# Kernel tuning notes

Measured on AMD Instinct MI355X. Metric: run time of the kernel, lower is better.

The kernel has to match this reference:

```python
import jax, jax.numpy as jnp
import numpy as np

N, E, F, H, ED, C, G = 50000, 800000, 86, 128, 16, 18, 64
NEG_SLOPE = 0.2


def setup_inputs() -> dict:
    key = jax.random.key(0)
    ks = jax.random.split(key, 20)
    s = 0.1
    return {
        "x": jax.random.normal(ks[0], (N, F), jnp.float32),
        "edge_index": jax.random.randint(ks[1], (2, E), 0, N, jnp.int32),
        "edge_attr": jax.random.normal(ks[2], (E, ED), jnp.float32),
        "batch": jnp.sort(jax.random.randint(ks[3], (N,), 0, G, jnp.int32)),
        # conv1 params (GATConv, heads=1): lin, lin_edge (no bias), att vectors, bias
        "W1": jax.random.normal(ks[4], (F, H), jnp.float32) * s,
        "We1": jax.random.normal(ks[5], (ED, H), jnp.float32) * s,
        "as1": jax.random.normal(ks[6], (H,), jnp.float32) * s,
        "ad1": jax.random.normal(ks[7], (H,), jnp.float32) * s,
        "ae1": jax.random.normal(ks[8], (H,), jnp.float32) * s,
        "b1": jnp.zeros((H,), jnp.float32),
        # conv2 params
        "W2": jax.random.normal(ks[9], (H, H), jnp.float32) * s,
        "We2": jax.random.normal(ks[10], (ED, H), jnp.float32) * s,
        "as2": jax.random.normal(ks[11], (H,), jnp.float32) * s,
        "ad2": jax.random.normal(ks[12], (H,), jnp.float32) * s,
        "ae2": jax.random.normal(ks[13], (H,), jnp.float32) * s,
        "b2": jnp.zeros((H,), jnp.float32),
        # final classifier
        "Wl": jax.random.normal(ks[14], (H, C), jnp.float32) * s,
        "bl": jnp.zeros((C,), jnp.float32),
    }


def gat_conv(x, edge_attr, src, dst, W, We, a_src, a_dst, a_edge, bias):
    h = x @ W                                   # [N, H]
    e = edge_attr @ We                          # [E, H]
    # per-edge attention logits: a_src.h_j + a_dst.h_i + a_edge.e
    alpha = (h @ a_src)[src] + (h @ a_dst)[dst] + e @ a_edge   # [E]
    alpha = jax.nn.leaky_relu(alpha, NEG_SLOPE)
    # segment softmax over incoming edges of each destination node
    m = jax.ops.segment_max(alpha, dst, num_segments=N)
    ex = jnp.exp(alpha - m[dst])
    denom = jax.ops.segment_sum(ex, dst, num_segments=N)
    w = ex / jnp.maximum(denom[dst], 1e-16)     # [E]
    out = jax.ops.segment_sum(h[src] * w[:, None], dst, num_segments=N)
    return out + bias


def reference(x, edge_index, edge_attr, batch,
              W1, We1, as1, ad1, ae1, b1,
              W2, We2, as2, ad2, ae2, b2,
              Wl, bl):
    src, dst = edge_index[0], edge_index[1]
    h = jax.nn.relu(gat_conv(x, edge_attr, src, dst, W1, We1, as1, ad1, ae1, b1))
    h = jax.nn.relu(gat_conv(h, edge_attr, src, dst, W2, We2, as2, ad2, ae2, b2))
    pooled = jax.ops.segment_max(h, batch, num_segments=G)      # [G, H] global max pool
    pooled = jnp.where(jnp.isfinite(pooled), pooled, 0.0)       # guard empty graphs
    logits = pooled @ Wl + bl                                   # [G, C]
    return jax.nn.log_softmax(logits, axis=-1)
```

## Files before the change

### kernel.cpp

```cpp
#include <hip/hip_runtime.h>
#include <math.h>

#define N_NODES 50000
#define N_EDGES 800000
#define F_IN    86
#define H_DIM   128
#define ED_DIM  16
#define C_CLS   18
#define G_GRAPHS 64
#define NEG_SLOPE 0.2f
#define SCAN_BLOCKS ((N_NODES + 255) / 256)

typedef _Float16 h2v   __attribute__((ext_vector_type(2)));
typedef _Float16 half8 __attribute__((ext_vector_type(8)));
typedef float    f4v   __attribute__((ext_vector_type(4)));

__device__ __forceinline__ void atomicMaxFloat(float* addr, float val) {
    if (val >= 0.0f) atomicMax((int*)addr, __float_as_int(val));
    else             atomicMin((unsigned int*)addr, __float_as_uint(val));
}

__global__ void prep(int* __restrict__ cnt, float* __restrict__ pooled,
                     const float* __restrict__ We1, const float* __restrict__ ae1,
                     const float* __restrict__ We2, const float* __restrict__ ae2,
                     float* __restrict__ ve1, float* __restrict__ ve2) {
    int b = blockIdx.x, t = threadIdx.x;
    if (b < SCAN_BLOCKS) {
        int i = b * 256 + t;
        if (i < N_NODES) cnt[i] = 0;
    } else {
        if (t < ED_DIM) {
            float s = 0.f;
            for (int h = 0; h < H_DIM; ++h) s += We1[t * H_DIM + h] * ae1[h];
            ve1[t] = s;
        } else if (t < 2 * ED_DIM) {
            int j = t - ED_DIM;
            float s = 0.f;
            for (int h = 0; h < H_DIM; ++h) s += We2[j * H_DIM + h] * ae2[h];
            ve2[j] = s;
        }
        for (int i = t; i < G_GRAPHS * H_DIM; i += 256) pooled[i] = 0.f;
    }
}

__global__ void hist_rank_dots(const int* __restrict__ dst, int* __restrict__ cnt,
                               unsigned short* __restrict__ rank,
                               const float* __restrict__ ea,
                               const float* __restrict__ ve1, const float* __restrict__ ve2,
                               unsigned int* __restrict__ dotp) {
    int e = blockIdx.x * blockDim.x + threadIdx.x;
    if (e >= N_EDGES) return;
    int r = atomicAdd(&cnt[dst[e]], 1);
    rank[e] = (unsigned short)r;
    const float4* p = (const float4*)(ea + (size_t)e * ED_DIM);
    float4 v0 = p[0], v1 = p[1], v2 = p[2], v3 = p[3];
    float s1 = v0.x*ve1[0] + v0.y*ve1[1] + v0.z*ve1[2] + v0.w*ve1[3]
             + v1.x*ve1[4] + v1.y*ve1[5] + v1.z*ve1[6] + v1.w*ve1[7]
             + v2.x*ve1[8] + v2.y*ve1[9] + v2.z*ve1[10] + v2.w*ve1[11]
             + v3.x*ve1[12] + v3.y*ve1[13] + v3.z*ve1[14] + v3.w*ve1[15];
    float s2 = v0.x*ve2[0] + v0.y*ve2[1] + v0.z*ve2[2] + v0.w*ve2[3]
             + v1.x*ve2[4] + v1.y*ve2[5] + v1.z*ve2[6] + v1.w*ve2[7]
             + v2.x*ve2[8] + v2.y*ve2[9] + v2.z*ve2[10] + v2.w*ve2[11]
             + v3.x*ve2[12] + v3.y*ve2[13] + v3.z*ve2[14] + v3.w*ve2[15];
    h2v dv;
    dv.x = (_Float16)s1;
    dv.y = (_Float16)s2;
    dotp[e] = __builtin_bit_cast(unsigned int, dv);
}

__global__ void scan1(const int* __restrict__ cnt, int* __restrict__ excl,
                      int* __restrict__ bsum) {
    __shared__ int s[256];
    int tid = threadIdx.x;
    int i = blockIdx.x * 256 + tid;
    int v = (i < N_NODES) ? cnt[i] : 0;
    s[tid] = v;
    __syncthreads();
    for (int o = 1; o < 256; o <<= 1) {
        int t = (tid >= o) ? s[tid - o] : 0;
        __syncthreads();
        s[tid] += t;
        __syncthreads();
    }
    if (i < N_NODES) excl[i] = s[tid] - v;
    if (tid == 255) bsum[blockIdx.x] = s[255];
}

__global__ void scan23(const int* __restrict__ excl, const int* __restrict__ bsum,
                       int* __restrict__ row_ptr) {
    __shared__ int s[256];
    int tid = threadIdx.x;
    int v = (tid < SCAN_BLOCKS) ? bsum[tid] : 0;
    s[tid] = v;
    __syncthreads();
    for (int o = 1; o < 256; o <<= 1) {
        int t = (tid >= o) ? s[tid - o] : 0;
        __syncthreads();
        s[tid] += t;
        __syncthreads();
    }
    int boff = s[blockIdx.x] - bsum[blockIdx.x];
    int i = blockIdx.x * 256 + tid;
    if (i < N_NODES) row_ptr[i] = excl[i] + boff;
    if (i == 0) row_ptr[N_NODES] = N_EDGES;
}

__global__ void scatter_lite(const int* __restrict__ src, const int* __restrict__ dst,
                             const int* __restrict__ row_ptr,
                             const unsigned short* __restrict__ rank,
                             const unsigned int* __restrict__ dotp,
                             int2* __restrict__ perm) {
    int e = blockIdx.x * blockDim.x + threadIdx.x;
    if (e >= N_EDGES) return;
    int pos = row_ptr[dst[e]] + rank[e];
    perm[pos] = make_int2(src[e], (int)dotp[e]);
}

#define KP1 104
__global__ __launch_bounds__(256)
void gemm1(const float* __restrict__ in, const float* __restrict__ W,
           const float* __restrict__ a_s, const float* __restrict__ a_d,
           _Float16* __restrict__ hout, float* __restrict__ hs, float* __restrict__ hd) {
    __shared__ __attribute__((aligned(16))) _Float16 Asm[64 * KP1];
    __shared__ __attribute__((aligned(16))) _Float16 Bsm[128 * KP1];
    __shared__ float sdots[64][2][2];
    int tid = threadIdx.x;
    int n0 = blockIdx.x * 64;

    const float2* in2 = (const float2*)(in + (size_t)n0 * F_IN);
    for (int idx = tid; idx < 64 * (F_IN / 2); idx += 256) {
        int r = idx / (F_IN / 2), k2 = idx - r * (F_IN / 2);
        float2 v = (n0 + r < N_NODES) ? in2[idx] : make_float2(0.f, 0.f);
        Asm[r * KP1 + 2 * k2]     = (_Float16)v.x;
        Asm[r * KP1 + 2 * k2 + 1] = (_Float16)v.y;
    }
    for (int idx = tid; idx < 64 * (96 - F_IN); idx += 256) {
        int r = idx / (96 - F_IN), k = F_IN + idx - r * (96 - F_IN);
        Asm[r * KP1 + k] = (_Float16)0.f;
    }
    const float4* W4 = (const float4*)W;
    for (int idx = tid; idx < F_IN * 32; idx += 256) {
        float4 v = W4[idx];
        int k = idx >> 5, n = (idx & 31) * 4;
        Bsm[(n + 0) * KP1 + k] = (_Float16)v.x;
        Bsm[(n + 1) * KP1 + k] = (_Float16)v.y;
        Bsm[(n + 2) * KP1 + k] = (_Float16)v.z;
        Bsm[(n + 3) * KP1 + k] = (_Float16)v.w;
    }
    for (int idx = tid; idx < 128 * (96 - F_IN); idx += 256) {
        int n = idx / (96 - F_IN), k = F_IN + idx - n * (96 - F_IN);
        Bsm[n * KP1 + k] = (_Float16)0.f;
    }
    __syncthreads();

    int wave = tid >> 6, lane = tid & 63;
    int wm = (wave & 1) * 32, wn = (wave >> 1) * 64;
    int m16 = lane & 15, quad = lane >> 4;

    f4v acc[2][4];
#pragma unroll
    for (int t = 0; t < 2; ++t)
#pragma unroll
        for (int c = 0; c < 4; ++c) acc[t][c] = (f4v){0.f, 0.f, 0.f, 0.f};

#pragma unroll
    for (int kk = 0; kk < 96 / 32; ++kk) {
        int koff = kk * 32 + quad * 8;
        half8 a0 = *(const half8*)&Asm[(wm + m16) * KP1 + koff];
        half8 a1 = *(const half8*)&Asm[(wm + 16 + m16) * KP1 + koff];
#pragma unroll
        for (int c = 0; c < 4; ++c) {
            half8 b = *(const half8*)&Bsm[(wn + c * 16 + m16) * KP1 + koff];
            acc[0][c] = __builtin_amdgcn_mfma_f32_16x16x32_f16(a0, b, acc[0][c], 0, 0, 0);
            acc[1][c] = __builtin_amdgcn_mfma_f32_16x16x32_f16(a1, b, acc[1][c], 0, 0, 0);
        }
    }

    float asv[4], adv[4];
#pragma unroll
    for (int c = 0; c < 4; ++c) {
        asv[c] = a_s[wn + c * 16 + m16];
        adv[c] = a_d[wn + c * 16 + m16];
    }
#pragma unroll
    for (int t = 0; t < 2; ++t)
#pragma unroll
        for (int r = 0; r < 4; ++r) {
            float ps = 0.f, pd = 0.f;
#pragma unroll
            for (int c = 0; c < 4; ++c) {
                float v = acc[t][c][r];
                ps += v * asv[c];
                pd += v * adv[c];
            }
#pragma unroll
            for (int o = 1; o < 16; o <<= 1) {
                ps += __shfl_xor(ps, o);
                pd += __shfl_xor(pd, o);
            }
            if (m16 == 0) {
                int row = wm + t * 16 + quad * 4 + r;
                sdots[row][wn >> 6][0] = ps;
                sdots[row][wn >> 6][1] = pd;
            }
        }
#pragma unroll
    for (int t = 0; t < 2; ++t)
#pragma unroll
        for (int c = 0; c < 4; ++c)
#pragma unroll
            for (int r = 0; r < 4; ++r) {
                int row = n0 + wm + t * 16 + quad * 4 + r;
                if (row < N_NODES)
                    hout[(size_t)row * H_DIM + wn + c * 16 + m16] = (_Float16)acc[t][c][r];
            }
    __syncthreads();
    if (tid < 64) {
        int row = n0 + tid;
        if (row < N_NODES) {
            hs[row] = sdots[tid][0][0] + sdots[tid][1][0];
            hd[row] = sdots[tid][0][1] + sdots[tid][1][1];
        }
    }
}

#define KP2 136
__global__ __launch_bounds__(256)
void gemm2(const _Float16* __restrict__ in, const float* __restrict__ W,
           const float* __restrict__ a_s, const float* __restrict__ a_d,
           _Float16* __restrict__ hout, float* __restrict__ hs, float* __restrict__ hd) {
    __shared__ __attribute__((aligned(16))) _Float16 Asm[64 * KP2];
    __shared__ __attribute__((aligned(16))) _Float16 Bsm[128 * KP2];
    __shared__ float sdots[64][2][2];
    int tid = threadIdx.x;
    int n0 = blockIdx.x * 64;

    const half8* in8 = (const half8*)(in + (size_t)n0 * H_DIM);
    for (int idx = tid; idx < 64 * 16; idx += 256) {
        int r = idx >> 4, k8 = idx & 15;
        half8 v = (n0 + r < N_NODES) ? in8[idx]
                                     : (half8){0, 0, 0, 0, 0, 0, 0, 0};
        *(half8*)&Asm[r * KP2 + k8 * 8] = v;
    }
    const float4* W4 = (const float4*)W;
    for (int idx = tid; idx < 128 * 32; idx += 256) {
        float4 v = W4[idx];
        int k = idx >> 5, n = (idx & 31) * 4;
        Bsm[(n + 0) * KP2 + k] = (_Float16)v.x;
        Bsm[(n + 1) * KP2 + k] = (_Float16)v.y;
        Bsm[(n + 2) * KP2 + k] = (_Float16)v.z;
        Bsm[(n + 3) * KP2 + k] = (_Float16)v.w;
    }
    __syncthreads();

    int wave = tid >> 6, lane = tid & 63;
    int wm = (wave & 1) * 32, wn = (wave >> 1) * 64;
    int m16 = lane & 15, quad = lane >> 4;

    f4v acc[2][4];
#pragma unroll
    for (int t = 0; t < 2; ++t)
#pragma unroll
        for (int c = 0; c < 4; ++c) acc[t][c] = (f4v){0.f, 0.f, 0.f, 0.f};

#pragma unroll
    for (int kk = 0; kk < 128 / 32; ++kk) {
        int koff = kk * 32 + quad * 8;
        half8 a0 = *(const half8*)&Asm[(wm + m16) * KP2 + koff];
        half8 a1 = *(const half8*)&Asm[(wm + 16 + m16) * KP2 + koff];
#pragma unroll
        for (int c = 0; c < 4; ++c) {
            half8 b = *(const half8*)&Bsm[(wn + c * 16 + m16) * KP2 + koff];
            acc[0][c] = __builtin_amdgcn_mfma_f32_16x16x32_f16(a0, b, acc[0][c], 0, 0, 0);
            acc[1][c] = __builtin_amdgcn_mfma_f32_16x16x32_f16(a1, b, acc[1][c], 0, 0, 0);
        }
    }

    float asv[4], adv[4];
#pragma unroll
    for (int c = 0; c < 4; ++c) {
        asv[c] = a_s[wn + c * 16 + m16];
        adv[c] = a_d[wn + c * 16 + m16];
    }
#pragma unroll
    for (int t = 0; t < 2; ++t)
#pragma unroll
        for (int r = 0; r < 4; ++r) {
            float ps = 0.f, pd = 0.f;
#pragma unroll
            for (int c = 0; c < 4; ++c) {
                float v = acc[t][c][r];
                ps += v * asv[c];
                pd += v * adv[c];
            }
#pragma unroll
            for (int o = 1; o < 16; o <<= 1) {
                ps += __shfl_xor(ps, o);
                pd += __shfl_xor(pd, o);
            }
            if (m16 == 0) {
                int row = wm + t * 16 + quad * 4 + r;
                sdots[row][wn >> 6][0] = ps;
                sdots[row][wn >> 6][1] = pd;
            }
        }
#pragma unroll
    for (int t = 0; t < 2; ++t)
#pragma unroll
        for (int c = 0; c < 4; ++c)
#pragma unroll
            for (int r = 0; r < 4; ++r) {
                int row = n0 + wm + t * 16 + quad * 4 + r;
                if (row < N_NODES)
                    hout[(size_t)row * H_DIM + wn + c * 16 + m16] = (_Float16)acc[t][c][r];
            }
    __syncthreads();
    if (tid < 64) {
        int row = n0 + tid;
        if (row < N_NODES) {
            hs[row] = sdots[tid][0][0] + sdots[tid][1][0];
            hd[row] = sdots[tid][0][1] + sdots[tid][1][1];
        }
    }
}

template<int DOT>
__global__ void gat_node(const int* __restrict__ row_ptr, const int2* __restrict__ perm,
                         const float* __restrict__ hs, const float* __restrict__ hd,
                         const _Float16* __restrict__ h, const float* __restrict__ bias,
                         _Float16* __restrict__ out) {
    int n = blockIdx.x * 4 + (threadIdx.x >> 6);
    int lane = threadIdx.x & 63;
    if (n >= N_NODES) return;
    int q = lane >> 4, m = lane & 15;
    int r0 = row_ptr[n], r1 = row_ptr[n + 1];
    float hdn = hd[n];

    float acc[8];
#pragma unroll
    for (int k = 0; k < 8; ++k) acc[k] = 0.f;
    float denl = 0.f;

    for (int c = r0; c < r1; c += 64) {
        int i = c + lane;
        float w = 0.f;
        int s = 0;
        if (i < r1) {
            int2 p = perm[i];
            s = p.x;
            h2v dv = __builtin_bit_cast(h2v, p.y);
            float dotv = (DOT == 1) ? (float)dv.x : (float)dv.y;
            float t = hs[s] + hdn + dotv;
            t = (t > 0.f) ? t : NEG_SLOPE * t;
            w = __expf(t);
        }
        denl += w;
        int lim = min(64, r1 - c);
        int njj = (lim + 7) >> 3;
        for (int jj = 0; jj < njj; ++jj) {
            int j1 = (jj << 3) + q;
            int j2 = j1 + 4;
            float w1 = __shfl(w, j1);
            int   s1 = __shfl(s, j1);
            float w2 = __shfl(w, j2);
            int   s2 = __shfl(s, j2);
            half8 v1 = *(const half8*)&h[(size_t)s1 * H_DIM + m * 8];
            half8 v2 = *(const half8*)&h[(size_t)s2 * H_DIM + m * 8];
#pragma unroll
            for (int k = 0; k < 8; ++k) acc[k] += w1 * (float)v1[k];
#pragma unroll
            for (int k = 0; k < 8; ++k) acc[k] += w2 * (float)v2[k];
        }
    }
#pragma unroll
    for (int k = 0; k < 8; ++k) {
        acc[k] += __shfl_xor(acc[k], 16);
        acc[k] += __shfl_xor(acc[k], 32);
    }
    float den = denl;
#pragma unroll
    for (int o = 32; o > 0; o >>= 1) den += __shfl_xor(den, o);
    float inv = 1.f / fmaxf(den, 1e-16f);

    if (q == 0) {
        float4 b0 = ((const float4*)bias)[2 * m];
        float4 b1 = ((const float4*)bias)[2 * m + 1];
        half8 ov;
        ov[0] = (_Float16)fmaxf(acc[0] * inv + b0.x, 0.f);
        ov[1] = (_Float16)fmaxf(acc[1] * inv + b0.y, 0.f);
        ov[2] = (_Float16)fmaxf(acc[2] * inv + b0.z, 0.f);
        ov[3] = (_Float16)fmaxf(acc[3] * inv + b0.w, 0.f);
        ov[4] = (_Float16)fmaxf(acc[4] * inv + b1.x, 0.f);
        ov[5] = (_Float16)fmaxf(acc[5] * inv + b1.y, 0.f);
        ov[6] = (_Float16)fmaxf(acc[6] * inv + b1.z, 0.f);
        ov[7] = (_Float16)fmaxf(acc[7] * inv + b1.w, 0.f);
        *(half8*)&out[(size_t)n * H_DIM + m * 8] = ov;
    }
}

__global__ void pool_max(const _Float16* __restrict__ P,
                         const int* __restrict__ batch, float* __restrict__ pooled) {
    int t = threadIdx.x;
    int n0 = blockIdx.x * 64;
    int n1 = min(n0 + 64, N_NODES);
    if (n0 >= N_NODES) return;
    int cur = batch[n0];
    float acc = 0.f;
    for (int n = n0; n < n1; ++n) {
        int g = batch[n];
        if (g != cur) {
            atomicMaxFloat(&pooled[cur * H_DIM + t], acc);
            acc = 0.f;
            cur = g;
        }
        acc = fmaxf(acc, (float)P[(size_t)n * H_DIM + t]);
    }
    atomicMaxFloat(&pooled[cur * H_DIM + t], acc);
}

__global__ void final_logits(const float* __restrict__ pooled, const float* __restrict__ Wl,
                             const float* __restrict__ bl, float* __restrict__ outp) {
    int g = threadIdx.x;
    if (g >= G_GRAPHS) return;
    float lg[C_CLS];
#pragma unroll
    for (int c = 0; c < C_CLS; ++c) lg[c] = bl[c];
    for (int k = 0; k < H_DIM; ++k) {
        float v = pooled[g * H_DIM + k];
#pragma unroll
        for (int c = 0; c < C_CLS; ++c) lg[c] += v * Wl[k * C_CLS + c];
    }
    float mx = lg[0];
#pragma unroll
    for (int c = 1; c < C_CLS; ++c) mx = fmaxf(mx, lg[c]);
    float se = 0.f;
#pragma unroll
    for (int c = 0; c < C_CLS; ++c) se += expf(lg[c] - mx);
    float lse = logf(se);
#pragma unroll
    for (int c = 0; c < C_CLS; ++c) outp[g * C_CLS + c] = lg[c] - mx - lse;
}

extern "C" void kernel_launch(void* const* d_in, const int* in_sizes, int n_in,
                              void* d_out, int out_size, void* d_ws, size_t ws_size,
                              hipStream_t stream) {
    const float* x     = (const float*)d_in[0];
    const int*   eidx  = (const int*)d_in[1];
    const float* ea    = (const float*)d_in[2];
    const int*   batch = (const int*)d_in[3];
    const float* W1  = (const float*)d_in[4];
    const float* We1 = (const float*)d_in[5];
    const float* as1 = (const float*)d_in[6];
    const float* ad1 = (const float*)d_in[7];
    const float* ae1 = (const float*)d_in[8];
    const float* b1  = (const float*)d_in[9];
    const float* W2  = (const float*)d_in[10];
    const float* We2 = (const float*)d_in[11];
    const float* as2 = (const float*)d_in[12];
    const float* ad2 = (const float*)d_in[13];
    const float* ae2 = (const float*)d_in[14];
    const float* b2  = (const float*)d_in[15];
    const float* Wl  = (const float*)d_in[16];
    const float* bl  = (const float*)d_in[17];
    float* outp = (float*)d_out;

    const int* src = eidx;
    const int* dst = eidx + N_EDGES;

    char* wsb = (char*)d_ws;
    size_t off = 0;
    auto alloc = [&](size_t bytes) { char* p = wsb + off; off += (bytes + 255) & ~(size_t)255; return p; };
    _Float16* h    = (_Float16*)alloc((size_t)N_NODES * H_DIM * 2);
    _Float16* A2   = (_Float16*)alloc((size_t)N_NODES * H_DIM * 2);
    _Float16* P    = (_Float16*)alloc((size_t)N_NODES * H_DIM * 2);
    int2*  perm    = (int2*)alloc((size_t)N_EDGES * 8);
    unsigned short* rank = (unsigned short*)alloc((size_t)N_EDGES * 2);
    unsigned int* dotp = (unsigned int*)alloc((size_t)N_EDGES * 4);
    float* hs      = (float*)alloc(N_NODES * 4);
    float* hd      = (float*)alloc(N_NODES * 4);
    int*   row_ptr = (int*)alloc((N_NODES + 1) * 4);
    int*   cnt     = (int*)alloc(N_NODES * 4);
    int*   excl    = (int*)alloc(N_NODES * 4);
    int*   bsum    = (int*)alloc(SCAN_BLOCKS * 4);
    float* pooled  = (float*)alloc(G_GRAPHS * H_DIM * 4);
    float* ve1     = (float*)alloc(16 * 4);
    float* ve2     = (float*)alloc(16 * 4);

    const int EB = (N_EDGES + 255) / 256;
    const int NB4 = (N_NODES + 3) / 4;
    const int GB = (N_NODES + 63) / 64;

    prep<<<SCAN_BLOCKS + 1, 256, 0, stream>>>(cnt, pooled, We1, ae1, We2, ae2, ve1, ve2);
    hist_rank_dots<<<EB, 256, 0, stream>>>(dst, cnt, rank, ea, ve1, ve2, dotp);
    scan1<<<SCAN_BLOCKS, 256, 0, stream>>>(cnt, excl, bsum);
    scan23<<<SCAN_BLOCKS, 256, 0, stream>>>(excl, bsum, row_ptr);
    scatter_lite<<<EB, 256, 0, stream>>>(src, dst, row_ptr, rank, dotp, perm);

    gemm1<<<GB, 256, 0, stream>>>(x, W1, as1, ad1, h, hs, hd);
    gat_node<1><<<NB4, 256, 0, stream>>>(row_ptr, perm, hs, hd, h, b1, A2);

    gemm2<<<GB, 256, 0, stream>>>(A2, W2, as2, ad2, h, hs, hd);
    gat_node<2><<<NB4, 256, 0, stream>>>(row_ptr, perm, hs, hd, h, b2, P);

    pool_max<<<GB, 128, 0, stream>>>(P, batch, pooled);
    final_logits<<<1, 64, 0, stream>>>(pooled, Wl, bl, outp);
}
```

Baseline: 342.2 us.

## Fuse gemm1 into histogram kernel and max-pool into second GAT aggregation

Merges the edge histogram/attention-dot kernel with the first node GEMM into a single launch, dispatching on block index so the two independent workloads share one grid. Fuses the global max pool into the second GAT node kernel: each block reduces its four nodes into shared memory and issues per-graph atomics. This removes the intermediate P buffer write/read and the separate pool kernel launch. The cost is extra syncs and shared atomics in gat_node, and a larger mixed kernel whose shared-memory footprint also applies to the edge blocks.

```diff
diff --git a/kernel.cpp b/kernel.cpp
--- a/kernel.cpp
+++ b/kernel.cpp
@@ -10,6 +10,8 @@
 #define G_GRAPHS 64
 #define NEG_SLOPE 0.2f
 #define SCAN_BLOCKS ((N_NODES + 255) / 256)
+#define EB_BLOCKS ((N_EDGES + 255) / 256)
+#define GB_BLOCKS ((N_NODES + 63) / 64)
 
 typedef _Float16 h2v   __attribute__((ext_vector_type(2)));
 typedef _Float16 half8 __attribute__((ext_vector_type(8)));
@@ -43,29 +45,139 @@
     }
 }
 
-__global__ void hist_rank_dots(const int* __restrict__ dst, int* __restrict__ cnt,
-                               unsigned short* __restrict__ rank,
-                               const float* __restrict__ ea,
-                               const float* __restrict__ ve1, const float* __restrict__ ve2,
-                               unsigned int* __restrict__ dotp) {
-    int e = blockIdx.x * blockDim.x + threadIdx.x;
-    if (e >= N_EDGES) return;
-    int r = atomicAdd(&cnt[dst[e]], 1);
-    rank[e] = (unsigned short)r;
-    const float4* p = (const float4*)(ea + (size_t)e * ED_DIM);
-    float4 v0 = p[0], v1 = p[1], v2 = p[2], v3 = p[3];
-    float s1 = v0.x*ve1[0] + v0.y*ve1[1] + v0.z*ve1[2] + v0.w*ve1[3]
-             + v1.x*ve1[4] + v1.y*ve1[5] + v1.z*ve1[6] + v1.w*ve1[7]
-             + v2.x*ve1[8] + v2.y*ve1[9] + v2.z*ve1[10] + v2.w*ve1[11]
-             + v3.x*ve1[12] + v3.y*ve1[13] + v3.z*ve1[14] + v3.w*ve1[15];
-    float s2 = v0.x*ve2[0] + v0.y*ve2[1] + v0.z*ve2[2] + v0.w*ve2[3]
-             + v1.x*ve2[4] + v1.y*ve2[5] + v1.z*ve2[6] + v1.w*ve2[7]
-             + v2.x*ve2[8] + v2.y*ve2[9] + v2.z*ve2[10] + v2.w*ve2[11]
-             + v3.x*ve2[12] + v3.y*ve2[13] + v3.z*ve2[14] + v3.w*ve2[15];
-    h2v dv;
-    dv.x = (_Float16)s1;
-    dv.y = (_Float16)s2;
-    dotp[e] = __builtin_bit_cast(unsigned int, dv);
+#define KP1 104
+__global__ __launch_bounds__(256)
+void hist_gemm1(const int* __restrict__ dst, int* __restrict__ cnt,
+                unsigned short* __restrict__ rank,
+                const float* __restrict__ ea,
+                const float* __restrict__ ve1, const float* __restrict__ ve2,
+                unsigned int* __restrict__ dotp,
+                const float* __restrict__ in, const float* __restrict__ W,
+                const float* __restrict__ a_s, const float* __restrict__ a_d,
+                _Float16* __restrict__ hout, float* __restrict__ hs,
+                float* __restrict__ hd) {
+    if (blockIdx.x < EB_BLOCKS) {
+        int e = blockIdx.x * 256 + threadIdx.x;
+        if (e >= N_EDGES) return;
+        int r = atomicAdd(&cnt[dst[e]], 1);
+        rank[e] = (unsigned short)r;
+        const float4* p = (const float4*)(ea + (size_t)e * ED_DIM);
+        float4 v0 = p[0], v1 = p[1], v2 = p[2], v3 = p[3];
+        float s1 = v0.x*ve1[0] + v0.y*ve1[1] + v0.z*ve1[2] + v0.w*ve1[3]
+                 + v1.x*ve1[4] + v1.y*ve1[5] + v1.z*ve1[6] + v1.w*ve1[7]
+                 + v2.x*ve1[8] + v2.y*ve1[9] + v2.z*ve1[10] + v2.w*ve1[11]
+                 + v3.x*ve1[12] + v3.y*ve1[13] + v3.z*ve1[14] + v3.w*ve1[15];
+        float s2 = v0.x*ve2[0] + v0.y*ve2[1] + v0.z*ve2[2] + v0.w*ve2[3]
+                 + v1.x*ve2[4] + v1.y*ve2[5] + v1.z*ve2[6] + v1.w*ve2[7]
+                 + v2.x*ve2[8] + v2.y*ve2[9] + v2.z*ve2[10] + v2.w*ve2[11]
+                 + v3.x*ve2[12] + v3.y*ve2[13] + v3.z*ve2[14] + v3.w*ve2[15];
+        h2v dv;
+        dv.x = (_Float16)s1;
+        dv.y = (_Float16)s2;
+        dotp[e] = __builtin_bit_cast(unsigned int, dv);
+        return;
+    }
+    __shared__ __attribute__((aligned(16))) _Float16 Asm[64 * KP1];
+    __shared__ __attribute__((aligned(16))) _Float16 Bsm[128 * KP1];
+    __shared__ float sdots[64][2][2];
+    int tid = threadIdx.x;
+    int n0 = (blockIdx.x - EB_BLOCKS) * 64;
+
+    const float2* in2 = (const float2*)(in + (size_t)n0 * F_IN);
+    for (int idx = tid; idx < 64 * (F_IN / 2); idx += 256) {
+        int r = idx / (F_IN / 2), k2 = idx - r * (F_IN / 2);
+        float2 v = (n0 + r < N_NODES) ? in2[idx] : make_float2(0.f, 0.f);
+        Asm[r * KP1 + 2 * k2]     = (_Float16)v.x;
+        Asm[r * KP1 + 2 * k2 + 1] = (_Float16)v.y;
+    }
+    for (int idx = tid; idx < 64 * (96 - F_IN); idx += 256) {
+        int r = idx / (96 - F_IN), k = F_IN + idx - r * (96 - F_IN);
+        Asm[r * KP1 + k] = (_Float16)0.f;
+    }
+    const float4* W4 = (const float4*)W;
+    for (int idx = tid; idx < F_IN * 32; idx += 256) {
+        float4 v = W4[idx];
+        int k = idx >> 5, n = (idx & 31) * 4;
+        Bsm[(n + 0) * KP1 + k] = (_Float16)v.x;
+        Bsm[(n + 1) * KP1 + k] = (_Float16)v.y;
+        Bsm[(n + 2) * KP1 + k] = (_Float16)v.z;
+        Bsm[(n + 3) * KP1 + k] = (_Float16)v.w;
+    }
+    for (int idx = tid; idx < 128 * (96 - F_IN); idx += 256) {
+        int n = idx / (96 - F_IN), k = F_IN + idx - n * (96 - F_IN);
+        Bsm[n * KP1 + k] = (_Float16)0.f;
+    }
+    __syncthreads();
+
+    int wave = tid >> 6, lane = tid & 63;
+    int wm = (wave & 1) * 32, wn = (wave >> 1) * 64;
+    int m16 = lane & 15, quad = lane >> 4;
+
+    f4v acc[2][4];
+#pragma unroll
+    for (int t = 0; t < 2; ++t)
+#pragma unroll
+        for (int c = 0; c < 4; ++c) acc[t][c] = (f4v){0.f, 0.f, 0.f, 0.f};
+
+#pragma unroll
+    for (int kk = 0; kk < 96 / 32; ++kk) {
+        int koff = kk * 32 + quad * 8;
+        half8 a0 = *(const half8*)&Asm[(wm + m16) * KP1 + koff];
+        half8 a1 = *(const half8*)&Asm[(wm + 16 + m16) * KP1 + koff];
+#pragma unroll
+        for (int c = 0; c < 4; ++c) {
+            half8 b = *(const half8*)&Bsm[(wn + c * 16 + m16) * KP1 + koff];
+            acc[0][c] = __builtin_amdgcn_mfma_f32_16x16x32_f16(a0, b, acc[0][c], 0, 0, 0);
+            acc[1][c] = __builtin_amdgcn_mfma_f32_16x16x32_f16(a1, b, acc[1][c], 0, 0, 0);
+        }
+    }
+
+    float asv[4], adv[4];
+#pragma unroll
+    for (int c = 0; c < 4; ++c) {
+        asv[c] = a_s[wn + c * 16 + m16];
+        adv[c] = a_d[wn + c * 16 + m16];
+    }
+#pragma unroll
+    for (int t = 0; t < 2; ++t)
+#pragma unroll
+        for (int r = 0; r < 4; ++r) {
+            float ps = 0.f, pd = 0.f;
+#pragma unroll
+            for (int c = 0; c < 4; ++c) {
+                float v = acc[t][c][r];
+                ps += v * asv[c];
+                pd += v * adv[c];
+            }
+#pragma unroll
+            for (int o = 1; o < 16; o <<= 1) {
+                ps += __shfl_xor(ps, o);
+                pd += __shfl_xor(pd, o);
+            }
+            if (m16 == 0) {
+                int row = wm + t * 16 + quad * 4 + r;
+                sdots[row][wn >> 6][0] = ps;
+                sdots[row][wn >> 6][1] = pd;
+            }
+        }
+#pragma unroll
+    for (int t = 0; t < 2; ++t)
+#pragma unroll
+        for (int c = 0; c < 4; ++c)
+#pragma unroll
+            for (int r = 0; r < 4; ++r) {
+                int row = n0 + wm + t * 16 + quad * 4 + r;
+                if (row < N_NODES)
+                    hout[(size_t)row * H_DIM + wn + c * 16 + m16] = (_Float16)acc[t][c][r];
+            }
+    __syncthreads();
+    if (tid < 64) {
+        int row = n0 + tid;
+        if (row < N_NODES) {
+            hs[row] = sdots[tid][0][0] + sdots[tid][1][0];
+            hd[row] = sdots[tid][0][1] + sdots[tid][1][1];
+        }
+    }
 }
 
 __global__ void scan1(const int* __restrict__ cnt, int* __restrict__ excl,
@@ -116,114 +228,6 @@
     perm[pos] = make_int2(src[e], (int)dotp[e]);
 }
 
-#define KP1 104
-__global__ __launch_bounds__(256)
-void gemm1(const float* __restrict__ in, const float* __restrict__ W,
-           const float* __restrict__ a_s, const float* __restrict__ a_d,
-           _Float16* __restrict__ hout, float* __restrict__ hs, float* __restrict__ hd) {
-    __shared__ __attribute__((aligned(16))) _Float16 Asm[64 * KP1];
-    __shared__ __attribute__((aligned(16))) _Float16 Bsm[128 * KP1];
-    __shared__ float sdots[64][2][2];
-    int tid = threadIdx.x;
-    int n0 = blockIdx.x * 64;
-
-    const float2* in2 = (const float2*)(in + (size_t)n0 * F_IN);
-    for (int idx = tid; idx < 64 * (F_IN / 2); idx += 256) {
-        int r = idx / (F_IN / 2), k2 = idx - r * (F_IN / 2);
-        float2 v = (n0 + r < N_NODES) ? in2[idx] : make_float2(0.f, 0.f);
-        Asm[r * KP1 + 2 * k2]     = (_Float16)v.x;
-        Asm[r * KP1 + 2 * k2 + 1] = (_Float16)v.y;
-    }
-    for (int idx = tid; idx < 64 * (96 - F_IN); idx += 256) {
-        int r = idx / (96 - F_IN), k = F_IN + idx - r * (96 - F_IN);
-        Asm[r * KP1 + k] = (_Float16)0.f;
-    }
-    const float4* W4 = (const float4*)W;
-    for (int idx = tid; idx < F_IN * 32; idx += 256) {
-        float4 v = W4[idx];
-        int k = idx >> 5, n = (idx & 31) * 4;
-        Bsm[(n + 0) * KP1 + k] = (_Float16)v.x;
-        Bsm[(n + 1) * KP1 + k] = (_Float16)v.y;
-        Bsm[(n + 2) * KP1 + k] = (_Float16)v.z;
-        Bsm[(n + 3) * KP1 + k] = (_Float16)v.w;
-    }
-    for (int idx = tid; idx < 128 * (96 - F_IN); idx += 256) {
-        int n = idx / (96 - F_IN), k = F_IN + idx - n * (96 - F_IN);
-        Bsm[n * KP1 + k] = (_Float16)0.f;
-    }
-    __syncthreads();
-
-    int wave = tid >> 6, lane = tid & 63;
-    int wm = (wave & 1) * 32, wn = (wave >> 1) * 64;
-    int m16 = lane & 15, quad = lane >> 4;
-
-    f4v acc[2][4];
-#pragma unroll
-    for (int t = 0; t < 2; ++t)
-#pragma unroll
-        for (int c = 0; c < 4; ++c) acc[t][c] = (f4v){0.f, 0.f, 0.f, 0.f};
-
-#pragma unroll
-    for (int kk = 0; kk < 96 / 32; ++kk) {
-        int koff = kk * 32 + quad * 8;
-        half8 a0 = *(const half8*)&Asm[(wm + m16) * KP1 + koff];
-        half8 a1 = *(const half8*)&Asm[(wm + 16 + m16) * KP1 + koff];
-#pragma unroll
-        for (int c = 0; c < 4; ++c) {
-            half8 b = *(const half8*)&Bsm[(wn + c * 16 + m16) * KP1 + koff];
-            acc[0][c] = __builtin_amdgcn_mfma_f32_16x16x32_f16(a0, b, acc[0][c], 0, 0, 0);
-            acc[1][c] = __builtin_amdgcn_mfma_f32_16x16x32_f16(a1, b, acc[1][c], 0, 0, 0);
-        }
-    }
-
-    float asv[4], adv[4];
-#pragma unroll
-    for (int c = 0; c < 4; ++c) {
-        asv[c] = a_s[wn + c * 16 + m16];
-        adv[c] = a_d[wn + c * 16 + m16];
-    }
-#pragma unroll
-    for (int t = 0; t < 2; ++t)
-#pragma unroll
-        for (int r = 0; r < 4; ++r) {
-            float ps = 0.f, pd = 0.f;
-#pragma unroll
-            for (int c = 0; c < 4; ++c) {
-                float v = acc[t][c][r];
-                ps += v * asv[c];
-                pd += v * adv[c];
-            }
-#pragma unroll
-            for (int o = 1; o < 16; o <<= 1) {
-                ps += __shfl_xor(ps, o);
-                pd += __shfl_xor(pd, o);
-            }
-            if (m16 == 0) {
-                int row = wm + t * 16 + quad * 4 + r;
-                sdots[row][wn >> 6][0] = ps;
-                sdots[row][wn >> 6][1] = pd;
-            }
-        }
-#pragma unroll
-    for (int t = 0; t < 2; ++t)
-#pragma unroll
-        for (int c = 0; c < 4; ++c)
-#pragma unroll
-            for (int r = 0; r < 4; ++r) {
-                int row = n0 + wm + t * 16 + quad * 4 + r;
-                if (row < N_NODES)
-                    hout[(size_t)row * H_DIM + wn + c * 16 + m16] = (_Float16)acc[t][c][r];
-            }
-    __syncthreads();
-    if (tid < 64) {
-        int row = n0 + tid;
-        if (row < N_NODES) {
-            hs[row] = sdots[tid][0][0] + sdots[tid][1][0];
-            hd[row] = sdots[tid][0][1] + sdots[tid][1][1];
-        }
-    }
-}
-
 #define KP2 136
 __global__ __launch_bounds__(256)
 void gemm2(const _Float16* __restrict__ in, const float* __restrict__ W,
@@ -324,14 +328,21 @@
     }
 }
 
-template<int DOT>
+template<int DOT, bool POOL>
 __global__ void gat_node(const int* __restrict__ row_ptr, const int2* __restrict__ perm,
                          const float* __restrict__ hs, const float* __restrict__ hd,
                          const _Float16* __restrict__ h, const float* __restrict__ bias,
-                         _Float16* __restrict__ out) {
-    int n = blockIdx.x * 4 + (threadIdx.x >> 6);
-    int lane = threadIdx.x & 63;
-    if (n >= N_NODES) return;
+                         _Float16* __restrict__ out,
+                         const int* __restrict__ batch, float* __restrict__ pooled) {
+    __shared__ float smax[H_DIM];
+    __shared__ int sg[4];
+    int tid = threadIdx.x;
+    if (POOL) {
+        if (tid < H_DIM) smax[tid] = 0.f;
+        __syncthreads();
+    }
+    int n = blockIdx.x * 4 + (tid >> 6);
+    int lane = tid & 63;
     int q = lane >> 4, m = lane & 15;
     int r0 = row_ptr[n], r1 = row_ptr[n + 1];
     float hdn = hd[n];
@@ -382,40 +393,47 @@
     for (int o = 32; o > 0; o >>= 1) den += __shfl_xor(den, o);
     float inv = 1.f / fmaxf(den, 1e-16f);
 
+    float rv[8];
     if (q == 0) {
         float4 b0 = ((const float4*)bias)[2 * m];
         float4 b1 = ((const float4*)bias)[2 * m + 1];
-        half8 ov;
-        ov[0] = (_Float16)fmaxf(acc[0] * inv + b0.x, 0.f);
-        ov[1] = (_Float16)fmaxf(acc[1] * inv + b0.y, 0.f);
-        ov[2] = (_Float16)fmaxf(acc[2] * inv + b0.z, 0.f);
-        ov[3] = (_Float16)fmaxf(acc[3] * inv + b0.w, 0.f);
-        ov[4] = (_Float16)fmaxf(acc[4] * inv + b1.x, 0.f);
-        ov[5] = (_Float16)fmaxf(acc[5] * inv + b1.y, 0.f);
-        ov[6] = (_Float16)fmaxf(acc[6] * inv + b1.z, 0.f);
-        ov[7] = (_Float16)fmaxf(acc[7] * inv + b1.w, 0.f);
-        *(half8*)&out[(size_t)n * H_DIM + m * 8] = ov;
-    }
-}
-
-__global__ void pool_max(const _Float16* __restrict__ P,
-                         const int* __restrict__ batch, float* __restrict__ pooled) {
-    int t = threadIdx.x;
-    int n0 = blockIdx.x * 64;
-    int n1 = min(n0 + 64, N_NODES);
-    if (n0 >= N_NODES) return;
-    int cur = batch[n0];
-    float acc = 0.f;
-    for (int n = n0; n < n1; ++n) {
+        rv[0] = fmaxf(acc[0] * inv + b0.x, 0.f);
+        rv[1] = fmaxf(acc[1] * inv + b0.y, 0.f);
+        rv[2] = fmaxf(acc[2] * inv + b0.z, 0.f);
+        rv[3] = fmaxf(acc[3] * inv + b0.w, 0.f);
+        rv[4] = fmaxf(acc[4] * inv + b1.x, 0.f);
+        rv[5] = fmaxf(acc[5] * inv + b1.y, 0.f);
+        rv[6] = fmaxf(acc[6] * inv + b1.z, 0.f);
+        rv[7] = fmaxf(acc[7] * inv + b1.w, 0.f);
+    }
+
+    if (!POOL) {
+        if (q == 0) {
+            half8 ov;
+#pragma unroll
+            for (int k = 0; k < 8; ++k) ov[k] = (_Float16)rv[k];
+            *(half8*)&out[(size_t)n * H_DIM + m * 8] = ov;
+        }
+    } else {
         int g = batch[n];
-        if (g != cur) {
-            atomicMaxFloat(&pooled[cur * H_DIM + t], acc);
-            acc = 0.f;
-            cur = g;
-        }
-        acc = fmaxf(acc, (float)P[(size_t)n * H_DIM + t]);
-    }
-    atomicMaxFloat(&pooled[cur * H_DIM + t], acc);
+        if (lane == 0) sg[tid >> 6] = g;
+        if (q == 0) {
+#pragma unroll
+            for (int k = 0; k < 8; ++k)
+                atomicMax((int*)&smax[m * 8 + k], __float_as_int(rv[k]));
+        }
+        __syncthreads();
+        if (sg[0] == sg[3]) {
+            if (tid < H_DIM)
+                atomicMaxFloat(&pooled[sg[0] * H_DIM + tid], smax[tid]);
+        } else {
+            if (q == 0) {
+#pragma unroll
+                for (int k = 0; k < 8; ++k)
+                    atomicMaxFloat(&pooled[g * H_DIM + m * 8 + k], rv[k]);
+            }
+        }
+    }
 }
 
 __global__ void final_logits(const float* __restrict__ pooled, const float* __restrict__ Wl,
@@ -472,7 +490,6 @@
     auto alloc = [&](size_t bytes) { char* p = wsb + off; off += (bytes + 255) & ~(size_t)255; return p; };
     _Float16* h    = (_Float16*)alloc((size_t)N_NODES * H_DIM * 2);
     _Float16* A2   = (_Float16*)alloc((size_t)N_NODES * H_DIM * 2);
-    _Float16* P    = (_Float16*)alloc((size_t)N_NODES * H_DIM * 2);
     int2*  perm    = (int2*)alloc((size_t)N_EDGES * 8);
     unsigned short* rank = (unsigned short*)alloc((size_t)N_EDGES * 2);
     unsigned int* dotp = (unsigned int*)alloc((size_t)N_EDGES * 4);
@@ -486,22 +503,21 @@
     float* ve1     = (float*)alloc(16 * 4);
     float* ve2     = (float*)alloc(16 * 4);
 
-    const int EB = (N_EDGES + 255) / 256;
     const int NB4 = (N_NODES + 3) / 4;
-    const int GB = (N_NODES + 63) / 64;
 
     prep<<<SCAN_BLOCKS + 1, 256, 0, stream>>>(cnt, pooled, We1, ae1, We2, ae2, ve1, ve2);
-    hist_rank_dots<<<EB, 256, 0, stream>>>(dst, cnt, rank, ea, ve1, ve2, dotp);
+    hist_gemm1<<<EB_BLOCKS + GB_BLOCKS, 256, 0, stream>>>(dst, cnt, rank, ea, ve1, ve2,
+                                                          dotp, x, W1, as1, ad1, h, hs, hd);
     scan1<<<SCAN_BLOCKS, 256, 0, stream>>>(cnt, excl, bsum);
     scan23<<<SCAN_BLOCKS, 256, 0, stream>>>(excl, bsum, row_ptr);
-    scatter_lite<<<EB, 256, 0, stream>>>(src, dst, row_ptr, rank, dotp, perm);
-
-    gemm1<<<GB, 256, 0, stream>>>(x, W1, as1, ad1, h, hs, hd);
-    gat_node<1><<<NB4, 256, 0, stream>>>(row_ptr, perm, hs, hd, h, b1, A2);
-
-    gemm2<<<GB, 256, 0, stream>>>(A2, W2, as2, ad2, h, hs, hd);
-    gat_node<2><<<NB4, 256, 0, stream>>>(row_ptr, perm, hs, hd, h, b2, P);
-
-    pool_max<<<GB, 128, 0, stream>>>(P, batch, pooled);
+    scatter_lite<<<EB_BLOCKS, 256, 0, stream>>>(src, dst, row_ptr, rank, dotp, perm);
+
+    gat_node<1, false><<<NB4, 256, 0, stream>>>(row_ptr, perm, hs, hd, h, b1, A2,
+                                                batch, pooled);
+
+    gemm2<<<GB_BLOCKS, 256, 0, stream>>>(A2, W2, as2, ad2, h, hs, hd);
+    gat_node<2, true><<<NB4, 256, 0, stream>>>(row_ptr, perm, hs, hd, h, b2, nullptr,
+                                               batch, pooled);
+
     final_logits<<<1, 64, 0, stream>>>(pooled, Wl, bl, outp);
 }
```

Result: faster. 327.2 us (-4.4%).
